# Kernel optimization log

Measured on AMD Instinct MI355X. Metric: run time of the kernel, lower is better.

## Reference

```python
import jax, jax.numpy as jnp
import numpy as np

B, P, CD, RD, H, NR, OD, T = 1024, 22, 256, 64, 512, 12, 2, 100
IN = OD + 2 + CD + RD  # 324: [pos(2), ball(2), context(256), role_embed(64)]


def setup_inputs() -> dict:
    key = jax.random.key(0)
    ks = jax.random.split(key, 20)
    def n(k, shape, s=1.0):
        return jax.random.normal(k, shape, dtype=jnp.float32) * s
    sH = 1.0 / np.sqrt(H)
    sI = 1.0 / np.sqrt(IN)
    return {
        "context": n(ks[0], (B, P, CD)),
        "initial_position": n(ks[1], (B, P, OD)),
        "ball_landing": n(ks[2], (B, 2)),
        "roles": jax.random.randint(ks[3], (B, P), 0, NR, dtype=jnp.int32),
        "max_steps": T,
        "role_table": n(ks[4], (NR, RD), 0.02),
        # LSTM layer 0 (input_dim=IN)
        "W_ih0": n(ks[5], (4 * H, IN), sI),
        "W_hh0": n(ks[6], (4 * H, H), sH),
        "b0": n(ks[7], (4 * H,), sH),  # b_ih + b_hh fused
        # LSTM layer 1 (input_dim=H)
        "W_ih1": n(ks[8], (4 * H, H), sH),
        "W_hh1": n(ks[9], (4 * H, H), sH),
        "b1": n(ks[10], (4 * H,), sH),
        # output MLP: H -> H//2 -> OD
        "W_fc1": n(ks[11], (H // 2, H), sH),
        "b_fc1": n(ks[12], (H // 2,), sH),
        "W_fc2": n(ks[13], (OD, H // 2), 1.0 / np.sqrt(H // 2)),
        "b_fc2": n(ks[14], (OD,), 0.02),
        # initial_pos_encoder: Linear(OD, H)
        "W_init": n(ks[15], (H, OD), 1.0 / np.sqrt(OD)),
        "b_init": n(ks[16], (H,), 0.02),
    }


def _lstm_cell(x, h, c, W_ih, W_hh, b):
    # PyTorch gate order: i, f, g, o
    gates = x @ W_ih.T + h @ W_hh.T + b  # [N, 4H]
    i, f, g, o = jnp.split(gates, 4, axis=-1)
    c_new = jax.nn.sigmoid(f) * c + jax.nn.sigmoid(i) * jnp.tanh(g)
    h_new = jax.nn.sigmoid(o) * jnp.tanh(c_new)
    return h_new, c_new


def reference(context, initial_position, ball_landing, roles, max_steps,
              role_table, W_ih0, W_hh0, b0, W_ih1, W_hh1, b1,
              W_fc1, b_fc1, W_fc2, b_fc2, W_init, b_init):
    batch, num_players, context_dim = context.shape
    N = batch * num_players
    out_dim = initial_position.shape[-1]

    ctx_flat = context.reshape(N, context_dim)
    role_flat = role_table[roles].reshape(N, -1)
    ball_flat = jnp.broadcast_to(ball_landing[:, None, :], (batch, num_players, 2)).reshape(N, 2)
    static = jnp.concatenate([ball_flat, ctx_flat, role_flat], axis=1)  # [N, IN-2]

    pos0 = initial_position.reshape(N, out_dim)
    h0 = pos0 @ W_init.T + b_init  # initial_pos_encoder into layer-0 hidden
    c0 = jnp.zeros_like(h0)
    h1 = jnp.zeros_like(h0)
    c1 = jnp.zeros_like(h0)

    def step(carry, _):
        pos, h0, c0, h1, c1 = carry
        x = jnp.concatenate([pos, static], axis=1)  # [N, IN]
        h0, c0 = _lstm_cell(x, h0, c0, W_ih0, W_hh0, b0)
        h1, c1 = _lstm_cell(h0, h1, c1, W_ih1, W_hh1, b1)
        # output MLP (dropout inactive in eval)
        nxt = jax.nn.relu(h1 @ W_fc1.T + b_fc1) @ W_fc2.T + b_fc2  # [N, OD]
        return (nxt, h0, c0, h1, c1), nxt

    _, preds = jax.lax.scan(step, (pos0, h0, c0, h1, c1), None, length=max_steps)
    # preds: [T, N, OD] -> [batch, num_players, T, OD]
    preds = preds.transpose(1, 0, 2).reshape(batch, num_players, max_steps, out_dim)
    return preds
```

## Files before the change

kernel.cpp:

```cpp
#include <hip/hip_runtime.h>
#include <cstdint>


#define DEVI __device__ __forceinline__

typedef __bf16 bf16x8 __attribute__((ext_vector_type(8)));
typedef float  f32x4  __attribute__((ext_vector_type(4)));
typedef float  f32x2  __attribute__((ext_vector_type(2)));
typedef unsigned short u16x4 __attribute__((ext_vector_type(4)));

static constexpr int NROWS = 22528;
static constexpr int T_STEPS = 100;
static constexpr int NBM = 176;

DEVI unsigned short f2bf(float f) {
  unsigned u = __float_as_uint(f);
  u = u + 0x7FFFu + ((u >> 16) & 1u);
  return (unsigned short)(u >> 16);
}
DEVI float bf2f(unsigned short h) { return __uint_as_float(((unsigned)h) << 16); }

DEVI float fast_sigmoid(float x) {
  float e = __builtin_amdgcn_exp2f(-1.442695041f * x);
  return __builtin_amdgcn_rcpf(1.0f + e);
}
DEVI float fast_tanh(float x) {
  float e = __builtin_amdgcn_exp2f(2.885390082f * x);
  return 1.0f - 2.0f * __builtin_amdgcn_rcpf(e + 1.0f);
}

DEVI void async_copy16(const void* g, void* l) {
  __builtin_amdgcn_global_load_lds(
      (const __attribute__((address_space(1))) void*)g,
      (__attribute__((address_space(3))) void*)l, 16, 0, 0);
}

template <int KITERS, int KSWITCH>
DEVI void gemm_core(const unsigned short* __restrict__ A1, int lda1,
                    const unsigned short* __restrict__ A2, int lda2,
                    const unsigned short* __restrict__ B1, int ldb1,
                    const unsigned short* __restrict__ B2, int ldb2,
                    unsigned short* lds, f32x4 acc[4][4], int tid) {
  const int lane = tid & 63, wid = tid >> 6;
  const int wm = wid & 1, wn = wid >> 1;
  const int c16 = lane & 15, q = lane >> 4;
#pragma unroll
  for (int i = 0; i < 4; ++i)
#pragma unroll
    for (int j = 0; j < 4; ++j) acc[i][j] = f32x4{0.f, 0.f, 0.f, 0.f};
#pragma unroll
  for (int kt = 0; kt < KITERS; ++kt) {
    const bool sec = (kt >= KSWITCH);
    const unsigned short* Ab = sec ? A2 : A1;
    const unsigned short* Bb = sec ? B2 : B1;
    const int lda = sec ? lda2 : lda1;
    const int ldb = sec ? ldb2 : ldb1;
    const int kk = (sec ? (kt - KSWITCH) : kt) * 64;
    __syncthreads();
#pragma unroll
    for (int rd = 0; rd < 4; ++rd) {
      int p = rd * 256 + tid;
      int row = p >> 3, u = p & 7, ch = u ^ (row & 7);
      async_copy16(Ab + row * lda + kk + ch * 8, lds + p * 8);
      async_copy16(Bb + row * ldb + kk + ch * 8, lds + 8192 + p * 8);
    }
    __syncthreads();
#pragma unroll
    for (int s = 0; s < 2; ++s) {
      bf16x8 a[4], b[4];
#pragma unroll
      for (int mf = 0; mf < 4; ++mf) {
        int row = wm * 64 + mf * 16 + c16;
        int slot = row * 8 + ((s * 4 + q) ^ (row & 7));
        a[mf] = *(const bf16x8*)(lds + slot * 8);
      }
#pragma unroll
      for (int nf = 0; nf < 4; ++nf) {
        int row = wn * 64 + nf * 16 + c16;
        int slot = row * 8 + ((s * 4 + q) ^ (row & 7));
        b[nf] = *(const bf16x8*)(lds + 8192 + slot * 8);
      }
#pragma unroll
      for (int mf = 0; mf < 4; ++mf)
#pragma unroll
        for (int nf = 0; nf < 4; ++nf)
          acc[mf][nf] = __builtin_amdgcn_mfma_f32_16x16x32_bf16(a[mf], b[nf], acc[mf][nf], 0, 0, 0);
    }
  }
}

DEVI int orig_row(int j) {
  int tile = j >> 7, rem = j & 127;
  int half = rem >> 6, g = (rem >> 4) & 3, cc = rem & 15;
  return g * 512 + (tile * 32 + half * 16 + cc);
}

__global__ void k_prep_w(const float* __restrict__ Whh0, const float* __restrict__ Wih1,
                         const float* __restrict__ Whh1, const float* __restrict__ Wih0,
                         const float* __restrict__ Wfc1, const float* __restrict__ b0,
                         const float* __restrict__ b1,
                         unsigned short* __restrict__ W0p, unsigned short* __restrict__ Wc1p,
                         unsigned short* __restrict__ Wsp, unsigned short* __restrict__ Wfc1b,
                         float* __restrict__ Wposx, float* __restrict__ Wposy,
                         float* __restrict__ b0p4, float* __restrict__ b1p4) {
  int j = blockIdx.x;
  int k = threadIdx.x;
  int o = orig_row(j);
  W0p[j * 512 + k]         = f2bf(Whh0[o * 512 + k]);
  Wc1p[j * 1024 + k]       = f2bf(Wih1[o * 512 + k]);
  Wc1p[j * 1024 + 512 + k] = f2bf(Whh1[o * 512 + k]);
  if (k < 384) Wsp[j * 384 + k] = (k < 322) ? f2bf(Wih0[o * 324 + 2 + k]) : (unsigned short)0;
  if (k == 0) {
    int g = (j >> 4) & 3;
    int cg = (j >> 7) * 32 + ((j >> 6) & 1) * 16 + (j & 15);
    Wposx[cg * 4 + g] = Wih0[o * 324 + 0];
    Wposy[cg * 4 + g] = Wih0[o * 324 + 1];
    b0p4[cg * 4 + g] = b0[o];
    b1p4[cg * 4 + g] = b1[o];
  }
  if (j < 256) Wfc1b[j * 512 + k] = f2bf(Wfc1[j * 512 + k]);
}

__global__ void k_init_xs(const float* __restrict__ ball, const float* __restrict__ ctx,
                          const int* __restrict__ roles, const float* __restrict__ role_table,
                          unsigned short* __restrict__ Xs) {
  int n = blockIdx.x, col = threadIdx.x;
  int b = n / 22;
  float v;
  if (col < 2)        v = ball[b * 2 + col];
  else if (col < 258) v = ctx[(size_t)n * 256 + col - 2];
  else if (col < 322) v = role_table[roles[n] * 64 + col - 258];
  else                v = 0.f;
  Xs[(size_t)n * 384 + col] = f2bf(v);
}

__global__ void k_init_state(const float* __restrict__ pos0, const float* __restrict__ Winit,
                             const float* __restrict__ binit, unsigned short* __restrict__ Hcat,
                             float* __restrict__ c0, float* __restrict__ c1,
                             float* __restrict__ posb) {
  int idx = blockIdx.x * 256 + threadIdx.x;
  if (idx >= NROWS * 512) return;
  int n = idx >> 9, c = idx & 511;
  float px = pos0[n * 2 + 0], py = pos0[n * 2 + 1];
  float h0 = binit[c] + Winit[c * 2 + 0] * px + Winit[c * 2 + 1] * py;
  Hcat[(size_t)n * 1024 + c] = f2bf(h0);
  Hcat[(size_t)n * 1024 + 512 + c] = 0;
  c0[idx] = 0.f;
  c1[idx] = 0.f;
  if (c < 2) posb[n * 2 + c] = pos0[n * 2 + c];
}

__global__ __launch_bounds__(256) void k_static(const unsigned short* __restrict__ Xs,
                                                const unsigned short* __restrict__ Wsp,
                                                const float* __restrict__ b0p4,
                                                unsigned short* __restrict__ SP2) {
  __shared__ __align__(16) unsigned short lds[16384];
  int tid = threadIdx.x, bn = blockIdx.x, bm = blockIdx.y;
  f32x4 acc[4][4];
  const unsigned short* Ab = Xs + (size_t)bm * 128 * 384;
  const unsigned short* Bb = Wsp + (size_t)bn * 128 * 384;
  gemm_core<6, 6>(Ab, 384, Ab, 384, Bb, 384, Bb, 384, lds, acc, tid);
  int lane = tid & 63, wid = tid >> 6, wm = wid & 1, wn = wid >> 1;
  int c16 = lane & 15, q = lane >> 4;
  int cg = bn * 32 + wn * 16 + c16;
  f32x4 bb = *(const f32x4*)&b0p4[cg * 4];
#pragma unroll
  for (int mf = 0; mf < 4; ++mf) {
    int row0 = bm * 128 + wm * 64 + mf * 16 + q * 4;
#pragma unroll
    for (int r = 0; r < 4; ++r) {
      u16x4 v;
      v.x = f2bf(acc[mf][0][r] + bb.x);
      v.y = f2bf(acc[mf][1][r] + bb.y);
      v.z = f2bf(acc[mf][2][r] + bb.z);
      v.w = f2bf(acc[mf][3][r] + bb.w);
      ((u16x4*)SP2)[(size_t)(row0 + r) * 512 + cg] = v;
    }
  }
}


struct GemmSrc {
  const unsigned short *A1, *A2, *B1, *B2;
  int ldA1, ldA2, ldB1, ldB2;
};

template <int KT, int KSW>
DEVI void stage_q(const GemmSrc& g, int t, int s, int isB, unsigned short* dst, int tid) {
  int tt = (t >= KT) ? (t - 2) : t;
  const bool sec = (tt >= KSW);
  const unsigned short* base;
  int ld;
  if (isB) { base = sec ? g.B2 : g.B1; ld = sec ? g.ldB2 : g.ldB1; }
  else     { base = sec ? g.A2 : g.A1; ld = sec ? g.ldA2 : g.ldA1; }
  base += (sec ? (tt - KSW) : tt) * 64 + s * 32;
#pragma unroll
  for (int rd = 0; rd < 2; ++rd) {
    int p = rd * 512 + tid;
    int row = p >> 2, u = p & 3, ch = u ^ ((row >> 1) & 3);
    async_copy16(base + row * ld + ch * 8, dst + p * 8);
  }
}

#define GBAR   asm volatile("s_barrier" ::: "memory")
#define VMCNT4 asm volatile("s_waitcnt vmcnt(4)" ::: "memory")

template <int KT, int KSW>
DEVI void gemm8(const GemmSrc& g, unsigned short* lds, f32x4 acc[8][4], int tid) {
  const int lane = tid & 63, wid = tid >> 6;
  const int wm = wid >> 2, wn = wid & 3;
  const int c16 = lane & 15, q = lane >> 4;
#pragma unroll
  for (int i = 0; i < 8; ++i)
#pragma unroll
    for (int j = 0; j < 4; ++j) acc[i][j] = f32x4{0.f, 0.f, 0.f, 0.f};
  unsigned short* A00 = lds;
  unsigned short* A01 = lds + 8192;
  unsigned short* B00 = lds + 16384;
  unsigned short* B01 = lds + 24576;
  unsigned short* A10 = lds + 32768;
  unsigned short* A11 = lds + 40960;
  unsigned short* B10 = lds + 49152;
  unsigned short* B11 = lds + 57344;
  const int rowA0 = wm * 128 + c16;
  const int rowB0 = wn * 64 + c16;
  stage_q<KT, KSW>(g, 0, 0, 0, A00, tid);
  stage_q<KT, KSW>(g, 0, 0, 1, B00, tid);
  stage_q<KT, KSW>(g, 0, 1, 0, A01, tid);
  stage_q<KT, KSW>(g, 0, 1, 1, B01, tid);
  stage_q<KT, KSW>(g, 1, 0, 0, A10, tid);
  stage_q<KT, KSW>(g, 1, 0, 1, B10, tid);
  VMCNT4;
  GBAR;
  bf16x8 a[4], b[4];

#define LOADA(BASE, MG)                                                        \
  _Pragma("unroll")                                                            \
  for (int f = 0; f < 4; ++f) {                                                \
    int row = rowA0 + ((MG) * 4 + f) * 16;                                     \
    a[f] = *(const bf16x8*)((BASE) + (row * 4 + (q ^ ((row >> 1) & 3))) * 8);  \
  }
#define LOADB(BASE)                                                            \
  _Pragma("unroll")                                                            \
  for (int f = 0; f < 4; ++f) {                                                \
    int row = rowB0 + f * 16;                                                  \
    b[f] = *(const bf16x8*)((BASE) + (row * 4 + (q ^ ((row >> 1) & 3))) * 8);  \
  }
#define MFG(MG)                                                                \
  __builtin_amdgcn_s_setprio(1);                                               \
  _Pragma("unroll")                                                            \
  for (int f = 0; f < 4; ++f)                                                  \
    _Pragma("unroll")                                                          \
    for (int nf = 0; nf < 4; ++nf)                                             \
      acc[(MG) * 4 + f][nf] = __builtin_amdgcn_mfma_f32_16x16x32_bf16(         \
          a[f], b[nf], acc[(MG) * 4 + f][nf], 0, 0, 0);                        \
  __builtin_amdgcn_s_setprio(0);                                               \
  __builtin_amdgcn_sched_barrier(0);

#pragma unroll 1
  for (int it = 0; it < KT / 2; ++it) {
    const int t0 = 2 * it;
    LOADA(A00, 0); LOADB(B00);
    stage_q<KT, KSW>(g, t0 + 1, 1, 0, A11, tid);
    GBAR; MFG(0); GBAR;
    LOADA(A00, 1);
    stage_q<KT, KSW>(g, t0 + 1, 1, 1, B11, tid);
    GBAR; MFG(1); GBAR;
    LOADA(A01, 0); LOADB(B01);
    stage_q<KT, KSW>(g, t0 + 2, 0, 0, A00, tid);
    GBAR; MFG(0); GBAR;
    LOADA(A01, 1);
    stage_q<KT, KSW>(g, t0 + 2, 0, 1, B00, tid);
    GBAR; MFG(1); VMCNT4; GBAR;
    LOADA(A10, 0); LOADB(B10);
    stage_q<KT, KSW>(g, t0 + 2, 1, 0, A01, tid);
    GBAR; MFG(0); GBAR;
    LOADA(A10, 1);
    stage_q<KT, KSW>(g, t0 + 2, 1, 1, B01, tid);
    GBAR; MFG(1); GBAR;
    LOADA(A11, 0); LOADB(B11);
    stage_q<KT, KSW>(g, t0 + 3, 0, 0, A10, tid);
    GBAR; MFG(0); GBAR;
    LOADA(A11, 1);
    stage_q<KT, KSW>(g, t0 + 3, 0, 1, B10, tid);
    GBAR; MFG(1); VMCNT4; GBAR;
  }
  asm volatile("s_waitcnt vmcnt(0)" ::: "memory");
#undef LOADA
#undef LOADB
#undef MFG
}

DEVI void swz704(int l, int& bn, int& bm) {
  int xcd = l & 7, ii = l >> 3;
  bn = ii & 7;
  bm = (ii >> 3) * 8 + xcd;
}

template <bool USE_SP>
__global__ __launch_bounds__(512, 2) void k_s1_8(const unsigned short* __restrict__ cur,
                                                 const unsigned short* __restrict__ Xs,
                                                 const unsigned short* __restrict__ W0p,
                                                 const unsigned short* __restrict__ Wsp,
                                                 const unsigned short* __restrict__ SP2,
                                                 const float* __restrict__ b0p4,
                                                 const float* __restrict__ Wposx,
                                                 const float* __restrict__ Wposy,
                                                 const float* __restrict__ posb,
                                                 float* __restrict__ c0,
                                                 unsigned short* __restrict__ nxt) {
  __shared__ __align__(16) unsigned short lds[65536];
  const int tid = threadIdx.x;
  int bn, bm;
  swz704(blockIdx.x, bn, bm);
  f32x4 acc[8][4];
  GemmSrc g;
  g.A1 = cur + (size_t)bm * 256 * 1024; g.ldA1 = 1024;
  g.B1 = W0p + (size_t)bn * 256 * 512;  g.ldB1 = 512;
  if constexpr (USE_SP) {
    g.A2 = g.A1; g.ldA2 = 1024; g.B2 = g.B1; g.ldB2 = 512;
    gemm8<8, 8>(g, lds, acc, tid);
  } else {
    g.A2 = Xs + (size_t)bm * 256 * 384;  g.ldA2 = 384;
    g.B2 = Wsp + (size_t)bn * 256 * 384; g.ldB2 = 384;
    gemm8<14, 8>(g, lds, acc, tid);
  }
  const int lane = tid & 63, wid = tid >> 6;
  const int wm = wid >> 2, wn = wid & 3;
  const int c16 = lane & 15, q = lane >> 4;
  const int cg = bn * 64 + (wn >> 1) * 32 + (wn & 1) * 16 + c16;
  f32x4 wpx = *(const f32x4*)&Wposx[cg * 4];
  f32x4 wpy = *(const f32x4*)&Wposy[cg * 4];
  f32x4 sb = f32x4{0.f, 0.f, 0.f, 0.f};
  if constexpr (!USE_SP) sb = *(const f32x4*)&b0p4[cg * 4];
#pragma unroll
  for (int mf = 0; mf < 8; ++mf) {
    int row0 = bm * 256 + wm * 128 + mf * 16 + q * 4;
    f32x4 cold = *(const f32x4*)&c0[(size_t)cg * NROWS + row0];
    f32x4 cnew;
#pragma unroll
    for (int r = 0; r < 4; ++r) {
      size_t row = row0 + r;
      f32x2 pv = *(const f32x2*)&posb[row * 2];
      float s0 = sb.x, s1 = sb.y, s2 = sb.z, s3 = sb.w;
      if constexpr (USE_SP) {
        u16x4 sp = ((const u16x4*)SP2)[row * 512 + cg];
        s0 = bf2f(sp.x); s1 = bf2f(sp.y); s2 = bf2f(sp.z); s3 = bf2f(sp.w);
      }
      float gi = acc[mf][0][r] + s0 + pv.x * wpx.x + pv.y * wpy.x;
      float gf = acc[mf][1][r] + s1 + pv.x * wpx.y + pv.y * wpy.y;
      float gg = acc[mf][2][r] + s2 + pv.x * wpx.z + pv.y * wpy.z;
      float go = acc[mf][3][r] + s3 + pv.x * wpx.w + pv.y * wpy.w;
      float cn = fast_sigmoid(gf) * cold[r] + fast_sigmoid(gi) * fast_tanh(gg);
      cnew[r] = cn;
      nxt[row * 1024 + cg] = f2bf(fast_sigmoid(go) * fast_tanh(cn));
    }
    *(f32x4*)&c0[(size_t)cg * NROWS + row0] = cnew;
  }
}

__global__ __launch_bounds__(512, 2) void k_s2_8(const unsigned short* __restrict__ nxt_in,
                                                 const unsigned short* __restrict__ cur,
                                                 const unsigned short* __restrict__ Wc1p,
                                                 const float* __restrict__ b1p4,
                                                 float* __restrict__ c1,
                                                 unsigned short* __restrict__ nxt_out) {
  __shared__ __align__(16) unsigned short lds[65536];
  const int tid = threadIdx.x;
  int bn, bm;
  swz704(blockIdx.x, bn, bm);
  f32x4 acc[8][4];
  GemmSrc g;
  g.A1 = nxt_in + (size_t)bm * 256 * 1024;      g.ldA1 = 1024;
  g.A2 = cur + (size_t)bm * 256 * 1024 + 512;   g.ldA2 = 1024;
  g.B1 = Wc1p + (size_t)bn * 256 * 1024;        g.ldB1 = 1024;
  g.B2 = g.B1 + 512;                            g.ldB2 = 1024;
  gemm8<16, 8>(g, lds, acc, tid);
  const int lane = tid & 63, wid = tid >> 6;
  const int wm = wid >> 2, wn = wid & 3;
  const int c16 = lane & 15, q = lane >> 4;
  const int cg = bn * 64 + (wn >> 1) * 32 + (wn & 1) * 16 + c16;
  f32x4 bv = *(const f32x4*)&b1p4[cg * 4];
#pragma unroll
  for (int mf = 0; mf < 8; ++mf) {
    int row0 = bm * 256 + wm * 128 + mf * 16 + q * 4;
    f32x4 cold = *(const f32x4*)&c1[(size_t)cg * NROWS + row0];
    f32x4 cnew;
#pragma unroll
    for (int r = 0; r < 4; ++r) {
      size_t row = row0 + r;
      float gi = acc[mf][0][r] + bv.x;
      float gf = acc[mf][1][r] + bv.y;
      float gg = acc[mf][2][r] + bv.z;
      float go = acc[mf][3][r] + bv.w;
      float cn = fast_sigmoid(gf) * cold[r] + fast_sigmoid(gi) * fast_tanh(gg);
      cnew[r] = cn;
      nxt_out[row * 1024 + 512 + cg] = f2bf(fast_sigmoid(go) * fast_tanh(cn));
    }
    *(f32x4*)&c1[(size_t)cg * NROWS + row0] = cnew;
  }
}

__global__ __launch_bounds__(256) void k_s3(const unsigned short* __restrict__ H,
                                            const unsigned short* __restrict__ Wfc1b,
                                            const float* __restrict__ bfc1,
                                            const float* __restrict__ Wfc2,
                                            const float* __restrict__ bfc2,
                                            float* __restrict__ out, float* __restrict__ posb,
                                            int t) {
  __shared__ __align__(16) unsigned short ldsA[32 * 64];
  __shared__ __align__(16) unsigned short ldsB[256 * 64];
  __shared__ float wfc2s[512];
  __shared__ float red[32 * 8];
  int tid = threadIdx.x;
  int l = blockIdx.x, xcd = l & 7, i = l >> 3;
  int b32 = 4 * (xcd + 8 * (i >> 2)) + (i & 3);
  wfc2s[tid] = Wfc2[tid];
  wfc2s[tid + 256] = Wfc2[tid + 256];
  int lane = tid & 63, wid = tid >> 6;
  int c16 = lane & 15, q = lane >> 4;
  f32x4 acc[2][4];
#pragma unroll
  for (int ii = 0; ii < 2; ++ii)
#pragma unroll
    for (int jj = 0; jj < 4; ++jj) acc[ii][jj] = f32x4{0.f, 0.f, 0.f, 0.f};
  const unsigned short* Ab = H + (size_t)b32 * 32 * 1024 + 512;
#pragma unroll
  for (int kt = 0; kt < 8; ++kt) {
    int k0 = kt * 64;
    __syncthreads();
    {
      int p = tid;
      int row = p >> 3, u = p & 7, ch = u ^ (row & 7);
      async_copy16(Ab + row * 1024 + k0 + ch * 8, ldsA + p * 8);
    }
#pragma unroll
    for (int rd = 0; rd < 8; ++rd) {
      int p = rd * 256 + tid;
      int row = p >> 3, u = p & 7, ch = u ^ (row & 7);
      async_copy16(Wfc1b + row * 512 + k0 + ch * 8, ldsB + p * 8);
    }
    __syncthreads();
#pragma unroll
    for (int s = 0; s < 2; ++s) {
      bf16x8 a[2], b[4];
#pragma unroll
      for (int mf = 0; mf < 2; ++mf) {
        int row = mf * 16 + c16;
        int slot = row * 8 + ((s * 4 + q) ^ (row & 7));
        a[mf] = *(const bf16x8*)(ldsA + slot * 8);
      }
#pragma unroll
      for (int nf = 0; nf < 4; ++nf) {
        int row = wid * 64 + nf * 16 + c16;
        int slot = row * 8 + ((s * 4 + q) ^ (row & 7));
        b[nf] = *(const bf16x8*)(ldsB + slot * 8);
      }
#pragma unroll
      for (int mf = 0; mf < 2; ++mf)
#pragma unroll
        for (int nf = 0; nf < 4; ++nf)
          acc[mf][nf] = __builtin_amdgcn_mfma_f32_16x16x32_bf16(a[mf], b[nf], acc[mf][nf], 0, 0, 0);
    }
  }
  float part[2][2][4];
#pragma unroll
  for (int d = 0; d < 2; ++d)
#pragma unroll
    for (int mf = 0; mf < 2; ++mf)
#pragma unroll
      for (int r = 0; r < 4; ++r) part[d][mf][r] = 0.f;
#pragma unroll
  for (int nf = 0; nf < 4; ++nf) {
    int col = wid * 64 + nf * 16 + c16;
    float w0 = wfc2s[col], w1 = wfc2s[256 + col], bv = bfc1[col];
#pragma unroll
    for (int mf = 0; mf < 2; ++mf)
#pragma unroll
      for (int r = 0; r < 4; ++r) {
        float v = acc[mf][nf][r] + bv;
        v = v > 0.f ? v : 0.f;
        part[0][mf][r] += v * w0;
        part[1][mf][r] += v * w1;
      }
  }
#pragma unroll
  for (int st = 1; st < 16; st <<= 1)
#pragma unroll
    for (int d = 0; d < 2; ++d)
#pragma unroll
      for (int mf = 0; mf < 2; ++mf)
#pragma unroll
        for (int r = 0; r < 4; ++r)
          part[d][mf][r] += __shfl_xor(part[d][mf][r], st, 64);
  if (c16 == 0) {
#pragma unroll
    for (int mf = 0; mf < 2; ++mf)
#pragma unroll
      for (int r = 0; r < 4; ++r) {
        int rl = mf * 16 + q * 4 + r;
        red[rl * 8 + wid * 2 + 0] = part[0][mf][r];
        red[rl * 8 + wid * 2 + 1] = part[1][mf][r];
      }
  }
  __syncthreads();
  if (tid < 64) {
    int rl = tid >> 1, d = tid & 1;
    float s = red[rl * 8 + d] + red[rl * 8 + 2 + d] + red[rl * 8 + 4 + d]
            + red[rl * 8 + 6 + d] + bfc2[d];
    int rg = b32 * 32 + rl;
    out[((size_t)rg * T_STEPS + t) * 2 + d] = s;
    posb[rg * 2 + d] = s;
  }
}

extern "C" void kernel_launch(void* const* d_in, const int* in_sizes, int n_in,
                              void* d_out, int out_size, void* d_ws, size_t ws_size,
                              hipStream_t stream) {
  (void)in_sizes; (void)n_in; (void)out_size;
  const float* ctx   = (const float*)d_in[0];
  const float* pos0  = (const float*)d_in[1];
  const float* ball  = (const float*)d_in[2];
  const int*   roles = (const int*)d_in[3];
  const float* role_table = (const float*)d_in[5];
  const float* Wih0 = (const float*)d_in[6];
  const float* Whh0 = (const float*)d_in[7];
  const float* b0   = (const float*)d_in[8];
  const float* Wih1 = (const float*)d_in[9];
  const float* Whh1 = (const float*)d_in[10];
  const float* b1   = (const float*)d_in[11];
  const float* Wfc1 = (const float*)d_in[12];
  const float* bfc1 = (const float*)d_in[13];
  const float* Wfc2 = (const float*)d_in[14];
  const float* bfc2 = (const float*)d_in[15];
  const float* Winit = (const float*)d_in[16];
  const float* binit = (const float*)d_in[17];
  float* out = (float*)d_out;

  char* w = (char*)d_ws;
  size_t used = 0;
  auto alloc = [&](size_t bytes) {
    char* p = w + used;
    used += (bytes + 255) & ~(size_t)255;
    return p;
  };
  unsigned short* W0p   = (unsigned short*)alloc((size_t)2048 * 512 * 2);
  unsigned short* Wc1p  = (unsigned short*)alloc((size_t)2048 * 1024 * 2);
  unsigned short* Wfc1b = (unsigned short*)alloc((size_t)256 * 512 * 2);
  float* Wposx = (float*)alloc(2048 * 4);
  float* Wposy = (float*)alloc(2048 * 4);
  float* b0p4  = (float*)alloc(2048 * 4);
  float* b1p4  = (float*)alloc(2048 * 4);
  float* posb  = (float*)alloc((size_t)NROWS * 2 * 4);
  unsigned short* Hc0 = (unsigned short*)alloc((size_t)NROWS * 1024 * 2);
  float* c0   = (float*)alloc((size_t)NROWS * 512 * 4);
  float* c1   = (float*)alloc((size_t)NROWS * 512 * 4);
  unsigned short* Hc1 = (unsigned short*)alloc((size_t)NROWS * 1024 * 2);

  const size_t SP_BYTES = (size_t)NROWS * 2048 * 2;
  const bool use_sp = (ws_size >= used + SP_BYTES + (1u << 20));

  unsigned short *Xs, *Wsp, *SP2;
  if (use_sp) {
    SP2 = (unsigned short*)alloc(SP_BYTES);
    Xs  = Hc1;
    Wsp = Hc1 + (size_t)NROWS * 384;
  } else {
    SP2 = Hc1;
    Xs  = (unsigned short*)alloc((size_t)NROWS * 384 * 2);
    Wsp = (unsigned short*)alloc((size_t)2048 * 384 * 2);
  }

  k_prep_w<<<2048, 512, 0, stream>>>(Whh0, Wih1, Whh1, Wih0, Wfc1, b0, b1,
                                     W0p, Wc1p, Wsp, Wfc1b, Wposx, Wposy, b0p4, b1p4);
  k_init_xs<<<NROWS, 384, 0, stream>>>(ball, ctx, roles, role_table, Xs);
  k_init_state<<<(NROWS * 512 + 255) / 256, 256, 0, stream>>>(pos0, Winit, binit, Hc0, c0, c1, posb);

  if (use_sp) {
    dim3 gs(16, NBM);
    k_static<<<gs, 256, 0, stream>>>(Xs, Wsp, b0p4, SP2);
  }

  for (int t = 0; t < T_STEPS; ++t) {
    unsigned short* cur = (t & 1) ? Hc1 : Hc0;
    unsigned short* nxt = (t & 1) ? Hc0 : Hc1;
    if (use_sp)
      k_s1_8<true><<<704, 512, 0, stream>>>(cur, Xs, W0p, Wsp, SP2, b0p4,
                                            Wposx, Wposy, posb, c0, nxt);
    else
      k_s1_8<false><<<704, 512, 0, stream>>>(cur, Xs, W0p, Wsp, SP2, b0p4,
                                             Wposx, Wposy, posb, c0, nxt);
    k_s2_8<<<704, 512, 0, stream>>>(nxt, cur, Wc1p, b1p4, c1, nxt);
    k_s3<<<704, 256, 0, stream>>>(nxt, Wfc1b, bfc1, Wfc2, bfc2, out, posb, t);
  }
}
```

Measured before the change: 21.78 ms.

## Replace per-step kernel launches with a persistent row-partitioned LSTM kernel

Replaces the 300 per-timestep launches (layer0, layer1, MLP) with one persistent kernel of 256 blocks. Each block owns 88 rows and loops over all timesteps and all gate tiles, so the recurrence needs no grid-wide synchronisation. The block's A rows are kept in LDS across the two k-steps while weight tiles stream through double buffers. The aim is to remove launch overhead and inter-kernel global round-trips of hidden state. In exchange, each block re-reads the full weight matrices every step, parallelism is limited to 256 blocks, and rows are padded to 22536.

```diff
diff --git a/kernel.cpp b/kernel.cpp
--- a/kernel.cpp
+++ b/kernel.cpp
@@ -8,8 +8,10 @@
 typedef float  f32x4  __attribute__((ext_vector_type(4)));
 typedef float  f32x2  __attribute__((ext_vector_type(2)));
 typedef unsigned short u16x4 __attribute__((ext_vector_type(4)));
+typedef unsigned short u16x8 __attribute__((ext_vector_type(8)));
 
 static constexpr int NROWS = 22528;
+static constexpr int NROWSP = 22536;
 static constexpr int T_STEPS = 100;
 static constexpr int NBM = 176;
 
@@ -34,6 +36,8 @@
       (const __attribute__((address_space(1))) void*)g,
       (__attribute__((address_space(3))) void*)l, 16, 0, 0);
 }
+
+#define GBAR   asm volatile("s_barrier" ::: "memory")
 
 template <int KITERS, int KSWITCH>
 DEVI void gemm_core(const unsigned short* __restrict__ A1, int lda1,
@@ -134,6 +138,28 @@
   Xs[(size_t)n * 384 + col] = f2bf(v);
 }
 
+__global__ void k_init_p(const float* __restrict__ pos0, const float* __restrict__ Winit,
+                         const float* __restrict__ binit,
+                         unsigned short* __restrict__ h0A, unsigned short* __restrict__ h1A,
+                         float* __restrict__ c0, float* __restrict__ c1,
+                         float* __restrict__ posb, unsigned short* __restrict__ SP2) {
+  int idx = blockIdx.x * 256 + threadIdx.x;
+  if (idx >= NROWSP * 512) return;
+  int n = idx >> 9, c = idx & 511;
+  if (n < NROWS) {
+    float px = pos0[n * 2 + 0], py = pos0[n * 2 + 1];
+    h0A[(size_t)n * 512 + c] = f2bf(binit[c] + Winit[c * 2 + 0] * px + Winit[c * 2 + 1] * py);
+    if (c < 2) posb[n * 2 + c] = pos0[n * 2 + c];
+  } else {
+    h0A[(size_t)n * 512 + c] = 0;
+    if (c < 2) posb[n * 2 + c] = 0.f;
+    ((unsigned long long*)SP2)[(size_t)n * 512 + c] = 0ull;
+  }
+  h1A[(size_t)n * 512 + c] = 0;
+  c0[idx] = 0.f;
+  c1[idx] = 0.f;
+}
+
 __global__ void k_init_state(const float* __restrict__ pos0, const float* __restrict__ Winit,
                              const float* __restrict__ binit, unsigned short* __restrict__ Hcat,
                              float* __restrict__ c0, float* __restrict__ c1,
@@ -180,6 +206,230 @@
 }
 
 
+DEVI void stageA_p(const unsigned short* As, int rowbase, int coff,
+                   unsigned short* dst, int tid) {
+#pragma unroll
+  for (int rd = 0; rd < 3; ++rd) {
+    int p = rd * 512 + tid;
+    int row = p >> 4, gp = p & 15;
+    async_copy16(As + (size_t)(rowbase + row) * 512 + coff + (gp ^ (row & 7)) * 8,
+                 dst + p * 8);
+  }
+}
+
+DEVI void stageB_p(const char* Bnt, int ldb, int koff, unsigned short* dst, int tid) {
+#pragma unroll
+  for (int ks = 0; ks < 2; ++ks)
+#pragma unroll
+    for (int rd = 0; rd < 2; ++rd) {
+      int p = rd * 512 + tid;
+      int j = p >> 2, u = p & 3, ch = u ^ ((j >> 1) & 3);
+      async_copy16(Bnt + (size_t)j * ldb + koff + ks * 64 + ch * 16,
+                   dst + ks * 8192 + p * 8);
+    }
+}
+
+template <int KT, int KSW>
+DEVI void gemm_p(const unsigned short* A1, const unsigned short* A2, int rowbase,
+                 const char* Bnt, int ldb,
+                 unsigned short* Abuf, unsigned short* Bbuf,
+                 f32x4 acc[3][4], int tid) {
+  const int lane = tid & 63, wid = tid >> 6;
+  const int wm = wid >> 2, wn = wid & 3;
+  const int c16 = lane & 15, q = lane >> 4;
+#pragma unroll
+  for (int i = 0; i < 3; ++i)
+#pragma unroll
+    for (int j = 0; j < 4; ++j) acc[i][j] = f32x4{0.f, 0.f, 0.f, 0.f};
+  stageA_p(A1, rowbase, 0, Abuf, tid);
+  stageB_p(Bnt, ldb, 0, Bbuf, tid);
+#pragma unroll
+  for (int kt = 0; kt < KT; ++kt) {
+    GBAR;
+    int nIss = 0;
+    if (kt + 1 < KT) { stageB_p(Bnt, ldb, (kt + 1) * 128, Bbuf + ((kt + 1) & 1) * 16384, tid); nIss += 4; }
+    if ((kt & 1) == 0 && (kt / 2 + 1) < KT / 2) {
+      int c = kt / 2 + 1;
+      const unsigned short* As = (c < KSW / 2) ? A1 : A2;
+      int coff = ((c < KSW / 2) ? c : (c - KSW / 2)) * 128;
+      stageA_p(As, rowbase, coff, Abuf + (c & 1) * 12288, tid);
+      nIss += 3;
+    }
+    if (nIss == 7)      asm volatile("s_waitcnt vmcnt(7)" ::: "memory");
+    else if (nIss == 4) asm volatile("s_waitcnt vmcnt(4)" ::: "memory");
+    else if (nIss == 3) asm volatile("s_waitcnt vmcnt(3)" ::: "memory");
+    else                asm volatile("s_waitcnt vmcnt(0)" ::: "memory");
+    GBAR;
+    const unsigned short* Ab = Abuf + ((kt >> 1) & 1) * 12288;
+    const unsigned short* Bb = Bbuf + (kt & 1) * 16384;
+#pragma unroll
+    for (int ks = 0; ks < 2; ++ks) {
+      bf16x8 a[3], b[4];
+#pragma unroll
+      for (int mf = 0; mf < 3; ++mf) {
+        int rl = wm * 48 + mf * 16 + c16;
+        int g = (kt & 1) * 8 + ks * 4 + q;
+        a[mf] = *(const bf16x8*)(Ab + rl * 128 + (g ^ (rl & 7)) * 8);
+      }
+#pragma unroll
+      for (int nf = 0; nf < 4; ++nf) {
+        int jl = wn * 64 + nf * 16 + c16;
+        b[nf] = *(const bf16x8*)(Bb + ks * 8192 + (jl * 4 + (q ^ ((jl >> 1) & 3))) * 8);
+      }
+      __builtin_amdgcn_s_setprio(1);
+#pragma unroll
+      for (int mf = 0; mf < 3; ++mf)
+#pragma unroll
+        for (int nf = 0; nf < 4; ++nf)
+          acc[mf][nf] = __builtin_amdgcn_mfma_f32_16x16x32_bf16(a[mf], b[nf], acc[mf][nf], 0, 0, 0);
+      __builtin_amdgcn_s_setprio(0);
+    }
+    __builtin_amdgcn_sched_barrier(0);
+  }
+}
+
+__global__ __launch_bounds__(512, 2) void k_persist(
+    const unsigned short* __restrict__ W0p, const unsigned short* __restrict__ Wc1p,
+    const unsigned short* __restrict__ Wfc1b, const unsigned short* __restrict__ SP2,
+    const float* __restrict__ b1p4,
+    const float* __restrict__ Wposx, const float* __restrict__ Wposy,
+    const float* __restrict__ bfc1, const float* __restrict__ Wfc2,
+    const float* __restrict__ bfc2,
+    unsigned short* __restrict__ h0A, unsigned short* __restrict__ h0B,
+    unsigned short* __restrict__ h1A, unsigned short* __restrict__ h1B,
+    float* __restrict__ c0, float* __restrict__ c1,
+    float* __restrict__ posb, float* __restrict__ out) {
+  __shared__ __align__(16) unsigned short Abuf[2 * 12288];
+  __shared__ __align__(16) unsigned short Bbuf[2 * 16384];
+  __shared__ float wfc2s[512];
+  __shared__ float red[96 * 8];
+  const int tid = threadIdx.x, blk = blockIdx.x;
+  const int lane = tid & 63, wid = tid >> 6;
+  const int wm = wid >> 2, wn = wid & 3;
+  const int c16 = lane & 15, q = lane >> 4;
+  const int rowbase = blk * 88;
+  wfc2s[tid] = Wfc2[tid];
+  __syncthreads();
+  f32x4 acc[3][4];
+#pragma unroll 1
+  for (int t = 0; t < T_STEPS; ++t) {
+    const unsigned short* h0p = (t & 1) ? h0B : h0A;
+    unsigned short*       h0n = (t & 1) ? h0A : h0B;
+    const unsigned short* h1p = (t & 1) ? h1B : h1A;
+    unsigned short*       h1n = (t & 1) ? h1A : h1B;
+#pragma unroll 1
+    for (int nt = 0; nt < 8; ++nt) {
+      gemm_p<8, 8>(h0p, h0p, rowbase, (const char*)W0p + (size_t)nt * 256 * 1024, 1024,
+                   Abuf, Bbuf, acc, tid);
+      const int cg = nt * 64 + (wn >> 1) * 32 + (wn & 1) * 16 + c16;
+      f32x4 wpx = *(const f32x4*)&Wposx[cg * 4];
+      f32x4 wpy = *(const f32x4*)&Wposy[cg * 4];
+#pragma unroll
+      for (int mf = 0; mf < 3; ++mf) {
+        int row0 = rowbase + wm * 48 + mf * 16 + q * 4;
+        f32x4 cold = *(const f32x4*)&c0[(size_t)cg * NROWSP + row0];
+        f32x4 cnew;
+#pragma unroll
+        for (int r = 0; r < 4; ++r) {
+          size_t row = row0 + r;
+          f32x2 pv = *(const f32x2*)&posb[row * 2];
+          u16x4 sp = ((const u16x4*)SP2)[row * 512 + cg];
+          float gi = acc[mf][0][r] + bf2f(sp.x) + pv.x * wpx.x + pv.y * wpy.x;
+          float gf = acc[mf][1][r] + bf2f(sp.y) + pv.x * wpx.y + pv.y * wpy.y;
+          float gg = acc[mf][2][r] + bf2f(sp.z) + pv.x * wpx.z + pv.y * wpy.z;
+          float go = acc[mf][3][r] + bf2f(sp.w) + pv.x * wpx.w + pv.y * wpy.w;
+          float cn = fast_sigmoid(gf) * cold[r] + fast_sigmoid(gi) * fast_tanh(gg);
+          cnew[r] = cn;
+          h0n[row * 512 + cg] = f2bf(fast_sigmoid(go) * fast_tanh(cn));
+        }
+        *(f32x4*)&c0[(size_t)cg * NROWSP + row0] = cnew;
+      }
+      __syncthreads();
+    }
+#pragma unroll 1
+    for (int nt = 0; nt < 8; ++nt) {
+      gemm_p<16, 8>(h0n, h1p, rowbase, (const char*)Wc1p + (size_t)nt * 256 * 2048, 2048,
+                    Abuf, Bbuf, acc, tid);
+      const int cg = nt * 64 + (wn >> 1) * 32 + (wn & 1) * 16 + c16;
+      f32x4 bv = *(const f32x4*)&b1p4[cg * 4];
+#pragma unroll
+      for (int mf = 0; mf < 3; ++mf) {
+        int row0 = rowbase + wm * 48 + mf * 16 + q * 4;
+        f32x4 cold = *(const f32x4*)&c1[(size_t)cg * NROWSP + row0];
+        f32x4 cnew;
+#pragma unroll
+        for (int r = 0; r < 4; ++r) {
+          size_t row = row0 + r;
+          float gi = acc[mf][0][r] + bv.x;
+          float gf = acc[mf][1][r] + bv.y;
+          float gg = acc[mf][2][r] + bv.z;
+          float go = acc[mf][3][r] + bv.w;
+          float cn = fast_sigmoid(gf) * cold[r] + fast_sigmoid(gi) * fast_tanh(gg);
+          cnew[r] = cn;
+          h1n[row * 512 + cg] = f2bf(fast_sigmoid(go) * fast_tanh(cn));
+        }
+        *(f32x4*)&c1[(size_t)cg * NROWSP + row0] = cnew;
+      }
+      __syncthreads();
+    }
+    {
+      gemm_p<8, 8>(h1n, h1n, rowbase, (const char*)Wfc1b, 1024, Abuf, Bbuf, acc, tid);
+      float part[2][3][4];
+#pragma unroll
+      for (int d = 0; d < 2; ++d)
+#pragma unroll
+        for (int mf = 0; mf < 3; ++mf)
+#pragma unroll
+          for (int r = 0; r < 4; ++r) part[d][mf][r] = 0.f;
+#pragma unroll
+      for (int nf = 0; nf < 4; ++nf) {
+        int col = wn * 64 + nf * 16 + c16;
+        float w0 = wfc2s[col], w1 = wfc2s[256 + col], bv = bfc1[col];
+#pragma unroll
+        for (int mf = 0; mf < 3; ++mf)
+#pragma unroll
+          for (int r = 0; r < 4; ++r) {
+            float v = acc[mf][nf][r] + bv;
+            v = v > 0.f ? v : 0.f;
+            part[0][mf][r] += v * w0;
+            part[1][mf][r] += v * w1;
+          }
+      }
+#pragma unroll
+      for (int st = 1; st < 16; st <<= 1)
+#pragma unroll
+        for (int d = 0; d < 2; ++d)
+#pragma unroll
+          for (int mf = 0; mf < 3; ++mf)
+#pragma unroll
+            for (int r = 0; r < 4; ++r)
+              part[d][mf][r] += __shfl_xor(part[d][mf][r], st, 64);
+      if (c16 == 0) {
+#pragma unroll
+        for (int mf = 0; mf < 3; ++mf)
+#pragma unroll
+          for (int r = 0; r < 4; ++r) {
+            int rl = wm * 48 + mf * 16 + q * 4 + r;
+            red[rl * 8 + wn * 2 + 0] = part[0][mf][r];
+            red[rl * 8 + wn * 2 + 1] = part[1][mf][r];
+          }
+      }
+      __syncthreads();
+      if (tid < 192) {
+        int rl = tid >> 1, d = tid & 1;
+        float s = red[rl * 8 + d] + red[rl * 8 + 2 + d] + red[rl * 8 + 4 + d]
+                + red[rl * 8 + 6 + d] + bfc2[d];
+        if (rl < 88) {
+          int rg = rowbase + rl;
+          out[((size_t)rg * T_STEPS + t) * 2 + d] = s;
+          posb[rg * 2 + d] = s;
+        }
+      }
+      __syncthreads();
+    }
+  }
+}
+
 struct GemmSrc {
   const unsigned short *A1, *A2, *B1, *B2;
   int ldA1, ldA2, ldB1, ldB2;
@@ -202,7 +452,6 @@
   }
 }
 
-#define GBAR   asm volatile("s_barrier" ::: "memory")
 #define VMCNT4 asm volatile("s_waitcnt vmcnt(4)" ::: "memory")
 
 template <int KT, int KSW>
@@ -233,7 +482,6 @@
   VMCNT4;
   GBAR;
   bf16x8 a[4], b[4];
-
 #define LOADA(BASE, MG)                                                        \
   _Pragma("unroll")                                                            \
   for (int f = 0; f < 4; ++f) {                                                \
@@ -256,7 +504,6 @@
           a[f], b[nf], acc[(MG) * 4 + f][nf], 0, 0, 0);                        \
   __builtin_amdgcn_s_setprio(0);                                               \
   __builtin_amdgcn_sched_barrier(0);
-
 #pragma unroll 1
   for (int it = 0; it < KT / 2; ++it) {
     const int t0 = 2 * it;
@@ -297,18 +544,16 @@
   bm = (ii >> 3) * 8 + xcd;
 }
 
-template <bool USE_SP>
-__global__ __launch_bounds__(512, 2) void k_s1_8(const unsigned short* __restrict__ cur,
-                                                 const unsigned short* __restrict__ Xs,
-                                                 const unsigned short* __restrict__ W0p,
-                                                 const unsigned short* __restrict__ Wsp,
-                                                 const unsigned short* __restrict__ SP2,
-                                                 const float* __restrict__ b0p4,
-                                                 const float* __restrict__ Wposx,
-                                                 const float* __restrict__ Wposy,
-                                                 const float* __restrict__ posb,
-                                                 float* __restrict__ c0,
-                                                 unsigned short* __restrict__ nxt) {
+__global__ __launch_bounds__(512, 2) void k_s1_lite(const unsigned short* __restrict__ cur,
+                                                    const unsigned short* __restrict__ Xs,
+                                                    const unsigned short* __restrict__ W0p,
+                                                    const unsigned short* __restrict__ Wsp,
+                                                    const float* __restrict__ b0p4,
+                                                    const float* __restrict__ Wposx,
+                                                    const float* __restrict__ Wposy,
+                                                    const float* __restrict__ posb,
+                                                    float* __restrict__ c0,
+                                                    unsigned short* __restrict__ nxt) {
   __shared__ __align__(16) unsigned short lds[65536];
   const int tid = threadIdx.x;
   int bn, bm;
@@ -317,22 +562,16 @@
   GemmSrc g;
   g.A1 = cur + (size_t)bm * 256 * 1024; g.ldA1 = 1024;
   g.B1 = W0p + (size_t)bn * 256 * 512;  g.ldB1 = 512;
-  if constexpr (USE_SP) {
-    g.A2 = g.A1; g.ldA2 = 1024; g.B2 = g.B1; g.ldB2 = 512;
-    gemm8<8, 8>(g, lds, acc, tid);
-  } else {
-    g.A2 = Xs + (size_t)bm * 256 * 384;  g.ldA2 = 384;
-    g.B2 = Wsp + (size_t)bn * 256 * 384; g.ldB2 = 384;
-    gemm8<14, 8>(g, lds, acc, tid);
-  }
+  g.A2 = Xs + (size_t)bm * 256 * 384;   g.ldA2 = 384;
+  g.B2 = Wsp + (size_t)bn * 256 * 384;  g.ldB2 = 384;
+  gemm8<14, 8>(g, lds, acc, tid);
   const int lane = tid & 63, wid = tid >> 6;
   const int wm = wid >> 2, wn = wid & 3;
   const int c16 = lane & 15, q = lane >> 4;
   const int cg = bn * 64 + (wn >> 1) * 32 + (wn & 1) * 16 + c16;
   f32x4 wpx = *(const f32x4*)&Wposx[cg * 4];
   f32x4 wpy = *(const f32x4*)&Wposy[cg * 4];
-  f32x4 sb = f32x4{0.f, 0.f, 0.f, 0.f};
-  if constexpr (!USE_SP) sb = *(const f32x4*)&b0p4[cg * 4];
+  f32x4 sb = *(const f32x4*)&b0p4[cg * 4];
 #pragma unroll
   for (int mf = 0; mf < 8; ++mf) {
     int row0 = bm * 256 + wm * 128 + mf * 16 + q * 4;
@@ -342,15 +581,10 @@
     for (int r = 0; r < 4; ++r) {
       size_t row = row0 + r;
       f32x2 pv = *(const f32x2*)&posb[row * 2];
-      float s0 = sb.x, s1 = sb.y, s2 = sb.z, s3 = sb.w;
-      if constexpr (USE_SP) {
-        u16x4 sp = ((const u16x4*)SP2)[row * 512 + cg];
-        s0 = bf2f(sp.x); s1 = bf2f(sp.y); s2 = bf2f(sp.z); s3 = bf2f(sp.w);
-      }
-      float gi = acc[mf][0][r] + s0 + pv.x * wpx.x + pv.y * wpy.x;
-      float gf = acc[mf][1][r] + s1 + pv.x * wpx.y + pv.y * wpy.y;
-      float gg = acc[mf][2][r] + s2 + pv.x * wpx.z + pv.y * wpy.z;
-      float go = acc[mf][3][r] + s3 + pv.x * wpx.w + pv.y * wpy.w;
+      float gi = acc[mf][0][r] + sb.x + pv.x * wpx.x + pv.y * wpy.x;
+      float gf = acc[mf][1][r] + sb.y + pv.x * wpx.y + pv.y * wpy.y;
+      float gg = acc[mf][2][r] + sb.z + pv.x * wpx.z + pv.y * wpy.z;
+      float go = acc[mf][3][r] + sb.w + pv.x * wpx.w + pv.y * wpy.w;
       float cn = fast_sigmoid(gf) * cold[r] + fast_sigmoid(gi) * fast_tanh(gg);
       cnew[r] = cn;
       nxt[row * 1024 + cg] = f2bf(fast_sigmoid(go) * fast_tanh(cn));
@@ -551,46 +785,59 @@
   float* Wposy = (float*)alloc(2048 * 4);
   float* b0p4  = (float*)alloc(2048 * 4);
   float* b1p4  = (float*)alloc(2048 * 4);
-  float* posb  = (float*)alloc((size_t)NROWS * 2 * 4);
-  unsigned short* Hc0 = (unsigned short*)alloc((size_t)NROWS * 1024 * 2);
-  float* c0   = (float*)alloc((size_t)NROWS * 512 * 4);
-  float* c1   = (float*)alloc((size_t)NROWS * 512 * 4);
-  unsigned short* Hc1 = (unsigned short*)alloc((size_t)NROWS * 1024 * 2);
-
-  const size_t SP_BYTES = (size_t)NROWS * 2048 * 2;
-  const bool use_sp = (ws_size >= used + SP_BYTES + (1u << 20));
-
-  unsigned short *Xs, *Wsp, *SP2;
-  if (use_sp) {
-    SP2 = (unsigned short*)alloc(SP_BYTES);
-    Xs  = Hc1;
-    Wsp = Hc1 + (size_t)NROWS * 384;
-  } else {
-    SP2 = Hc1;
-    Xs  = (unsigned short*)alloc((size_t)NROWS * 384 * 2);
-    Wsp = (unsigned short*)alloc((size_t)2048 * 384 * 2);
-  }
-
-  k_prep_w<<<2048, 512, 0, stream>>>(Whh0, Wih1, Whh1, Wih0, Wfc1, b0, b1,
-                                     W0p, Wc1p, Wsp, Wfc1b, Wposx, Wposy, b0p4, b1p4);
-  k_init_xs<<<NROWS, 384, 0, stream>>>(ball, ctx, roles, role_table, Xs);
-  k_init_state<<<(NROWS * 512 + 255) / 256, 256, 0, stream>>>(pos0, Winit, binit, Hc0, c0, c1, posb);
-
-  if (use_sp) {
+  float* posb  = (float*)alloc((size_t)NROWSP * 2 * 4);
+  unsigned short* h0A = (unsigned short*)alloc((size_t)NROWSP * 512 * 2);
+  unsigned short* h0B = (unsigned short*)alloc((size_t)NROWSP * 512 * 2);
+  unsigned short* h1A = (unsigned short*)alloc((size_t)NROWSP * 512 * 2);
+  unsigned short* h1B = (unsigned short*)alloc((size_t)NROWSP * 512 * 2);
+  float* c0   = (float*)alloc((size_t)512 * NROWSP * 4);
+  float* c1   = (float*)alloc((size_t)512 * NROWSP * 4);
+  unsigned short* SP2 = (unsigned short*)alloc((size_t)NROWSP * 2048 * 2);
+  unsigned short* Xs  = h0B;
+  unsigned short* Wsp = h1B;
+
+  const bool use_p = (ws_size >= used + (1u << 20));
+
+  if (use_p) {
+    k_prep_w<<<2048, 512, 0, stream>>>(Whh0, Wih1, Whh1, Wih0, Wfc1, b0, b1,
+                                       W0p, Wc1p, Wsp, Wfc1b, Wposx, Wposy, b0p4, b1p4);
+    k_init_xs<<<NROWS, 384, 0, stream>>>(ball, ctx, roles, role_table, Xs);
+    k_init_p<<<(NROWSP * 512 + 255) / 256, 256, 0, stream>>>(pos0, Winit, binit,
+                                                             h0A, h1A, c0, c1, posb, SP2);
     dim3 gs(16, NBM);
     k_static<<<gs, 256, 0, stream>>>(Xs, Wsp, b0p4, SP2);
-  }
-
-  for (int t = 0; t < T_STEPS; ++t) {
-    unsigned short* cur = (t & 1) ? Hc1 : Hc0;
-    unsigned short* nxt = (t & 1) ? Hc0 : Hc1;
-    if (use_sp)
-      k_s1_8<true><<<704, 512, 0, stream>>>(cur, Xs, W0p, Wsp, SP2, b0p4,
-                                            Wposx, Wposy, posb, c0, nxt);
-    else
-      k_s1_8<false><<<704, 512, 0, stream>>>(cur, Xs, W0p, Wsp, SP2, b0p4,
-                                             Wposx, Wposy, posb, c0, nxt);
-    k_s2_8<<<704, 512, 0, stream>>>(nxt, cur, Wc1p, b1p4, c1, nxt);
-    k_s3<<<704, 256, 0, stream>>>(nxt, Wfc1b, bfc1, Wfc2, bfc2, out, posb, t);
-  }
-}
+    k_persist<<<256, 512, 0, stream>>>(W0p, Wc1p, Wfc1b, SP2, b1p4, Wposx, Wposy,
+                                       bfc1, Wfc2, bfc2, h0A, h0B, h1A, h1B,
+                                       c0, c1, posb, out);
+  } else {
+    used = 0;
+    unsigned short* W0pL   = (unsigned short*)alloc((size_t)2048 * 512 * 2);
+    unsigned short* Wc1pL  = (unsigned short*)alloc((size_t)2048 * 1024 * 2);
+    unsigned short* Wfc1bL = (unsigned short*)alloc((size_t)256 * 512 * 2);
+    float* WposxL = (float*)alloc(2048 * 4);
+    float* WposyL = (float*)alloc(2048 * 4);
+    float* b0p4L  = (float*)alloc(2048 * 4);
+    float* b1p4L  = (float*)alloc(2048 * 4);
+    float* posbL  = (float*)alloc((size_t)NROWS * 2 * 4);
+    unsigned short* Hc0 = (unsigned short*)alloc((size_t)NROWS * 1024 * 2);
+    float* c0L   = (float*)alloc((size_t)NROWS * 512 * 4);
+    float* c1L   = (float*)alloc((size_t)NROWS * 512 * 4);
+    unsigned short* Hc1 = (unsigned short*)alloc((size_t)NROWS * 1024 * 2);
+    unsigned short* XsL  = (unsigned short*)alloc((size_t)NROWS * 384 * 2);
+    unsigned short* WspL = (unsigned short*)alloc((size_t)2048 * 384 * 2);
+
+    k_prep_w<<<2048, 512, 0, stream>>>(Whh0, Wih1, Whh1, Wih0, Wfc1, b0, b1,
+                                       W0pL, Wc1pL, WspL, Wfc1bL, WposxL, WposyL, b0p4L, b1p4L);
+    k_init_xs<<<NROWS, 384, 0, stream>>>(ball, ctx, roles, role_table, XsL);
+    k_init_state<<<(NROWS * 512 + 255) / 256, 256, 0, stream>>>(pos0, Winit, binit, Hc0,
+                                                                c0L, c1L, posbL);
+    for (int t = 0; t < T_STEPS; ++t) {
+      unsigned short* cur = (t & 1) ? Hc1 : Hc0;
+      unsigned short* nxt = (t & 1) ? Hc0 : Hc1;
+      k_s1_lite<<<704, 512, 0, stream>>>(cur, XsL, W0pL, WspL, b0p4L,
+                                         WposxL, WposyL, posbL, c0L, nxt);
+      k_s2_8<<<704, 512, 0, stream>>>(nxt, cur, Wc1pL, b1p4L, c1L, nxt);
+      k_s3<<<704, 256, 0, stream>>>(nxt, Wfc1bL, bfc1, Wfc2, bfc2, out, posbL, t);
+    }
+  }
+}
```

New measurement: 21.52 ms. No clear change (-1.2%).
